# Performance work log

Hardware: AMD Instinct MI355X
Metric: run time of the kernel (lower is better)

## Reference

```python
import jax, jax.numpy as jnp
import numpy as np

L = 64      # system size
H = 64      # hiddenSize
IN = 4      # inputDim (POVM)
B = 4096    # batch of configurations


def _make_w(k, din, dout):
    # Padded block-triangular weight: W[idx, i, j, s] is nonzero only for j >= idx,
    # matching Dense(features=(L-idx)*dout) output scattered into rows idx: of h.
    W = jax.random.normal(k, (L, din, L, dout), dtype=jnp.float32) / jnp.sqrt(jnp.float32(din))
    mask = (jnp.arange(L)[:, None] <= jnp.arange(L)[None, :]).astype(jnp.float32)  # [idx, j]
    return W * mask[:, None, :, None]


def setup_inputs() -> dict:
    key = jax.random.key(0)
    ks = jax.random.split(key, 7)
    x = jax.random.randint(ks[0], (B, L), 0, IN, dtype=jnp.int32)
    W0 = _make_w(ks[1], IN, H)
    W1 = _make_w(ks[2], H, H)
    W2 = _make_w(ks[3], H, 4)
    # bias exists only for site idx==0; its (L*size,) output reshaped to (L, size)
    # is added to all rows of h, so it acts as the initial value of h[d].
    b0 = 0.1 * jax.random.normal(ks[4], (L, H), dtype=jnp.float32)
    b1 = 0.1 * jax.random.normal(ks[5], (L, H), dtype=jnp.float32)
    b2 = 0.1 * jax.random.normal(ks[6], (L, 4), dtype=jnp.float32)
    return {"x": x, "W0": W0, "W1": W1, "W2": W2, "b0": b0, "b1": b1, "b2": b2}


def reference(x, W0, W1, W2, b0, b1, b2):
    Bn = x.shape[0]
    x_oh = jax.nn.one_hot(x, IN, dtype=jnp.float32)                      # (B, L, 4)
    # ffn_cell input: one-hot of x[:-1], shifted right with a zero row prepended
    x_in = jnp.concatenate([jnp.zeros((Bn, 1, IN), jnp.float32), x_oh[:, :-1]], axis=1)

    h0 = jnp.broadcast_to(b0, (Bn, L, H))
    h1 = jnp.broadcast_to(b1, (Bn, L, H))
    h2 = jnp.broadcast_to(b2, (Bn, L, 4))

    def step(carry, inp):
        h0, h1, h2 = carry
        a, idx, w0, w1, w2 = inp                                        # a: (B, 4)
        h0 = h0 + jnp.einsum('bi,ijs->bjs', a, w0)                      # scatter-add rows >= idx
        a = jax.nn.elu(jnp.take(h0, idx, axis=1))                       # (B, H)
        h1 = h1 + jnp.einsum('bi,ijs->bjs', a, w1)
        a = jax.nn.elu(jnp.take(h1, idx, axis=1))
        h2 = h2 + jnp.einsum('bi,ijs->bjs', a, w2)
        return (h0, h1, h2), None

    xs = (jnp.swapaxes(x_in, 0, 1), jnp.arange(L), W0, W1, W2)
    (h0, h1, h2), _ = jax.lax.scan(step, (h0, h1, h2), xs)

    out = jax.nn.elu(h2)                                                # (B, L, 4)
    logp = jnp.sum(jax.nn.log_softmax(out, axis=-1) * x_oh, axis=(1, 2))
    return logp                                                         # (B,)
```

## Files before the change

kernel.cpp:

```cpp
#include <hip/hip_runtime.h>
#include <hip/hip_bf16.h>

#define LL 64
#define HH 64
#define KDIM 4096

typedef __attribute__((ext_vector_type(8))) short bf16x8;
typedef __attribute__((ext_vector_type(4))) short s16x4;
typedef __attribute__((ext_vector_type(4))) float f32x4;

__device__ inline short f2bf(float f) {
    __hip_bfloat16 h = __float2bfloat16(f);
    return *reinterpret_cast<short*>(&h);
}
__device__ inline float elu1(float x) { return x > 0.f ? x : expm1f(x); }

__device__ inline void global_load_lds16(const short* g, short* l) {
    __builtin_amdgcn_global_load_lds(
        (const __attribute__((address_space(1))) unsigned int*)g,
        (__attribute__((address_space(3))) unsigned int*)l,
        16, 0, 0);
}

__global__ __launch_bounds__(256) void k_transpose_cvt(
    const float* __restrict__ in, short* __restrict__ out, int R, int C,
    int skip_margin)
{
    __shared__ float tile[32][33];
    int tx = threadIdx.x & 31, ty = threadIdx.x >> 5;
    size_t r0 = (size_t)blockIdx.y * 32, c0 = (size_t)blockIdx.x * 32;
    if (skip_margin >= 0 && (int)r0 >= (int)c0 + skip_margin) return;
#pragma unroll
    for (int i = 0; i < 32; i += 8)
        tile[ty + i][tx] = in[(r0 + ty + i) * C + (c0 + tx)];
    __syncthreads();
#pragma unroll
    for (int i = 0; i < 32; i += 8)
        out[(c0 + ty + i) * R + (r0 + tx)] = f2bf(tile[tx][ty + i]);
}

__global__ __launch_bounds__(256) void k_onehot(
    const int* __restrict__ x, short* __restrict__ Xoh)
{
    int b = blockIdx.x * 4 + (threadIdx.x >> 6);
    int t = threadIdx.x & 63;
    s16x4 v = {0, 0, 0, 0};
    if (t > 0) {
        int xi = x[b * LL + t - 1];
        v[xi] = (short)0x3F80;
    }
    *(s16x4*)(Xoh + (size_t)b * 256 + t * 4) = v;
}

template<int SHIFT, bool OUT_BF16>
__global__ __launch_bounds__(256) void k_gemm_bt(
    const short* __restrict__ A,
    const short* __restrict__ BT,
    const float* __restrict__ bias,
    void* __restrict__ Cv,
    int M, int N, int K)
{
    constexpr int BM = 128, BN = 128, BK = 32;
    __shared__ short As[BM * BK];
    __shared__ short Bs[BN * BK];

    int m0 = blockIdx.x * BM;
    int n0 = ((int)gridDim.y - 1 - (int)blockIdx.y) * BN;
    int tid = threadIdx.x;
    int wave = tid >> 6, lane = tid & 63;
    int wm = (wave >> 1) * 64, wn = (wave & 1) * 64;

    int ke;
    if constexpr (SHIFT >= 0) ke = (n0 + BN) << SHIFT;
    else                      ke = (n0 + BN) >> (-SHIFT);
    int k_end = min(K, ke);

    f32x4 acc[4][4] = {};

    int rsub = lane >> 2;
    int csub = (lane & 3) * 8;
    const short* ga = A  + (size_t)(m0 + wave * 16 + rsub) * K + csub;
    const short* gb = BT + (size_t)(n0 + wave * 16 + rsub) * K + csub;
    short* lA = &As[(wave * 16) * BK];
    short* lB = &Bs[(wave * 16) * BK];

    int lrow = lane & 15;
    int lko  = (lane >> 4) * 8;
    const short* rA = &As[(wm + lrow) * BK + lko];
    const short* rB = &Bs[(wn + lrow) * BK + lko];

    for (int kb = 0; kb < k_end; kb += BK) {
        __syncthreads();
        global_load_lds16(ga + kb,                  lA);
        global_load_lds16(ga + kb + (size_t)64 * K, lA + 64 * BK);
        global_load_lds16(gb + kb,                  lB);
        global_load_lds16(gb + kb + (size_t)64 * K, lB + 64 * BK);
        __syncthreads();

        bf16x8 af[4], bf[4];
#pragma unroll
        for (int i = 0; i < 4; ++i) {
            af[i] = *(const bf16x8*)(rA + i * 16 * BK);
            bf[i] = *(const bf16x8*)(rB + i * 16 * BK);
        }
#pragma unroll
        for (int mi = 0; mi < 4; ++mi)
#pragma unroll
            for (int ni = 0; ni < 4; ++ni)
                acc[mi][ni] = __builtin_amdgcn_mfma_f32_16x16x32_bf16(
                    af[mi], bf[ni], acc[mi][ni], 0, 0, 0);
    }

    int lcol = lane & 15;
    int lr4  = (lane >> 4) * 4;
#pragma unroll
    for (int mi = 0; mi < 4; ++mi) {
#pragma unroll
        for (int ni = 0; ni < 4; ++ni) {
            int col = n0 + wn + ni * 16 + lcol;
            float bv = bias[col];
#pragma unroll
            for (int r = 0; r < 4; ++r) {
                int row = m0 + wm + mi * 16 + lr4 + r;
                float v = elu1(acc[mi][ni][r] + bv);
                if (OUT_BF16) ((short*)Cv)[(size_t)row * N + col] = f2bf(v);
                else          ((float*)Cv)[(size_t)row * N + col] = v;
            }
        }
    }
}

template<int SHIFT, int ZSPLIT>
__global__ __launch_bounds__(256) void k_gemm_bt_splitk(
    const short* __restrict__ A, const short* __restrict__ BT,
    float* __restrict__ part, int M, int N, int K)
{
    constexpr int BM = 128, BN = 128, BK = 32;
    __shared__ short As[BM * BK];
    __shared__ short Bs[BN * BK];

    int m0 = blockIdx.x * BM;
    int n0 = ((int)gridDim.y - 1 - (int)blockIdx.y) * BN;
    int z = blockIdx.z;
    int tid = threadIdx.x;
    int wave = tid >> 6, lane = tid & 63;
    int wm = (wave >> 1) * 64, wn = (wave & 1) * 64;

    int k_end = min(K, (n0 + BN) << SHIFT);
    int chunk = ((k_end / ZSPLIT + BK - 1) / BK) * BK;
    int kb0 = z * chunk;
    int kb1 = min(k_end, kb0 + chunk);

    f32x4 acc[4][4] = {};

    int rsub = lane >> 2;
    int csub = (lane & 3) * 8;
    const short* ga = A  + (size_t)(m0 + wave * 16 + rsub) * K + csub;
    const short* gb = BT + (size_t)(n0 + wave * 16 + rsub) * K + csub;
    short* lA = &As[(wave * 16) * BK];
    short* lB = &Bs[(wave * 16) * BK];

    int lrow = lane & 15;
    int lko  = (lane >> 4) * 8;
    const short* rA = &As[(wm + lrow) * BK + lko];
    const short* rB = &Bs[(wn + lrow) * BK + lko];

    for (int kb = kb0; kb < kb1; kb += BK) {
        __syncthreads();
        global_load_lds16(ga + kb,                  lA);
        global_load_lds16(ga + kb + (size_t)64 * K, lA + 64 * BK);
        global_load_lds16(gb + kb,                  lB);
        global_load_lds16(gb + kb + (size_t)64 * K, lB + 64 * BK);
        __syncthreads();

        bf16x8 af[4], bf[4];
#pragma unroll
        for (int i = 0; i < 4; ++i) {
            af[i] = *(const bf16x8*)(rA + i * 16 * BK);
            bf[i] = *(const bf16x8*)(rB + i * 16 * BK);
        }
#pragma unroll
        for (int mi = 0; mi < 4; ++mi)
#pragma unroll
            for (int ni = 0; ni < 4; ++ni)
                acc[mi][ni] = __builtin_amdgcn_mfma_f32_16x16x32_bf16(
                    af[mi], bf[ni], acc[mi][ni], 0, 0, 0);
    }

    float* p = part + (size_t)z * M * N;
    int lcol = lane & 15;
    int lr4  = (lane >> 4) * 4;
#pragma unroll
    for (int mi = 0; mi < 4; ++mi)
#pragma unroll
        for (int ni = 0; ni < 4; ++ni) {
            int col = n0 + wn + ni * 16 + lcol;
#pragma unroll
            for (int r = 0; r < 4; ++r) {
                int row = m0 + wm + mi * 16 + lr4 + r;
                p[(size_t)row * N + col] = acc[mi][ni][r];
            }
        }
}

__global__ __launch_bounds__(256) void k_logp_fused(
    const float* __restrict__ part, const float* __restrict__ b2,
    const int* __restrict__ x, float* __restrict__ logp)
{
    const size_t MN = (size_t)4096 * 256;
    int b = blockIdx.x * 4 + (threadIdx.x >> 6);
    int j = threadIdx.x & 63;
    size_t idx = (size_t)b * 256 + j * 4;

    f32x4 o = *(const f32x4*)(part + idx);
    f32x4 p1 = *(const f32x4*)(part + idx + MN);
    f32x4 p2 = *(const f32x4*)(part + idx + 2 * MN);
    f32x4 p3 = *(const f32x4*)(part + idx + 3 * MN);
    f32x4 bv = *(const f32x4*)(b2 + j * 4);
#pragma unroll
    for (int s = 0; s < 4; ++s)
        o[s] = elu1(o[s] + p1[s] + p2[s] + p3[s] + bv[s]);

    float m = fmaxf(fmaxf(o[0], o[1]), fmaxf(o[2], o[3]));
    float lse = m + logf(expf(o[0] - m) + expf(o[1] - m) +
                         expf(o[2] - m) + expf(o[3] - m));
    int xi = x[b * LL + j];
    float sel = (xi == 0) ? o[0] : (xi == 1) ? o[1] : (xi == 2) ? o[2] : o[3];
    float c = sel - lse;
#pragma unroll
    for (int off = 32; off > 0; off >>= 1)
        c += __shfl_down(c, off, 64);
    if (j == 0) logp[b] = c;
}

extern "C" void kernel_launch(void* const* d_in, const int* in_sizes, int n_in,
                              void* d_out, int out_size, void* d_ws, size_t ws_size,
                              hipStream_t stream)
{
    const int*   x  = (const int*)  d_in[0];
    const float* W0 = (const float*)d_in[1];
    const float* W1 = (const float*)d_in[2];
    const float* W2 = (const float*)d_in[3];
    const float* b0 = (const float*)d_in[4];
    const float* b1 = (const float*)d_in[5];
    const float* b2 = (const float*)d_in[6];
    float* logp = (float*)d_out;

    char* ws = (char*)d_ws;
    short* W1T  = (short*)(ws);
    short* W2T  = (short*)(ws + (size_t)33554432);
    short* W0T  = (short*)(ws + (size_t)35651584);
    short* Xoh  = (short*)(ws + (size_t)37748736);
    short* A1   = (short*)(ws + (size_t)39845888);
    float* part = (float*)(ws + (size_t)39845888);
    short* A2   = (short*)(ws + (size_t)73400320);

    k_transpose_cvt<<<dim3(128, 128), 256, 0, stream>>>(W1, W1T, 4096, 4096, 160);
    k_transpose_cvt<<<dim3(8, 128),   256, 0, stream>>>(W2, W2T, 4096, 256, -1);
    k_transpose_cvt<<<dim3(128, 8),   256, 0, stream>>>(W0, W0T, 256, 4096, -1);

    k_onehot<<<1024, 256, 0, stream>>>(x, Xoh);

    k_gemm_bt<-4, true><<<dim3(32, 32), 256, 0, stream>>>(Xoh, W0T, b0, A1, 4096, 4096, 256);

    k_gemm_bt<0, true><<<dim3(32, 32), 256, 0, stream>>>(A1, W1T, b1, A2, 4096, 4096, 4096);

    k_gemm_bt_splitk<4, 4><<<dim3(32, 2, 4), 256, 0, stream>>>(A2, W2T, part, 4096, 256, 4096);

    k_logp_fused<<<1024, 256, 0, stream>>>(part, b2, x, logp);
}
```

Measured before the change: 182.7 us.

## Merge weight transposes into one launch and interleave triangular GEMM tile order

Replaces the three transpose-convert kernel launches with one launch that splits its flat block index across W1, W2 and W0, which removes per-launch overhead and tail gaps. It also remaps the GEMM's N-tile ordering through tri_map, interleaving heavy and light column tiles of the triangular workload so that concurrently scheduled blocks have more even K ranges. The remap only takes effect when the grid's y-dimension is a multiple of 8, and it adds integer division to each block's setup.

```diff
diff --git a/kernel.cpp b/kernel.cpp
--- a/kernel.cpp
+++ b/kernel.cpp
@@ -22,14 +22,38 @@
         16, 0, 0);
 }
 
-__global__ __launch_bounds__(256) void k_transpose_cvt(
-    const float* __restrict__ in, short* __restrict__ out, int R, int C,
-    int skip_margin)
-{
+__device__ inline int tri_map(int yy, int gy) {
+    if ((gy & 7) == 0) {
+        int q = gy >> 2, i = yy / q, r = yy % q;
+        return (i == 0) ? r
+             : (i == 1) ? (gy / 2 - 1 - r)
+             : (i == 2) ? (gy / 2 + r)
+                        : (gy - 1 - r);
+    }
+    return gy - 1 - yy;
+}
+
+__global__ __launch_bounds__(256) void k_transpose_all(
+    const float* __restrict__ W1, short* __restrict__ W1T,
+    const float* __restrict__ W2, short* __restrict__ W2T,
+    const float* __restrict__ W0, short* __restrict__ W0T)
+{
+    const float* in; short* out; int R, C, bx, by;
+    int bid = blockIdx.x;
+    if (bid < 16384) {
+        bx = bid & 127; by = bid >> 7;
+        if (by * 32 >= bx * 32 + 160) return;
+        in = W1; out = W1T; R = 4096; C = 4096;
+    } else if (bid < 17408) {
+        int id = bid - 16384; bx = id & 7; by = id >> 3;
+        in = W2; out = W2T; R = 4096; C = 256;
+    } else {
+        int id = bid - 17408; bx = id & 127; by = id >> 7;
+        in = W0; out = W0T; R = 256; C = 4096;
+    }
     __shared__ float tile[32][33];
     int tx = threadIdx.x & 31, ty = threadIdx.x >> 5;
-    size_t r0 = (size_t)blockIdx.y * 32, c0 = (size_t)blockIdx.x * 32;
-    if (skip_margin >= 0 && (int)r0 >= (int)c0 + skip_margin) return;
+    size_t r0 = (size_t)by * 32, c0 = (size_t)bx * 32;
 #pragma unroll
     for (int i = 0; i < 32; i += 8)
         tile[ty + i][tx] = in[(r0 + ty + i) * C + (c0 + tx)];
@@ -65,7 +89,7 @@
     __shared__ short Bs[BN * BK];
 
     int m0 = blockIdx.x * BM;
-    int n0 = ((int)gridDim.y - 1 - (int)blockIdx.y) * BN;
+    int n0 = tri_map(blockIdx.y, gridDim.y) * BN;
     int tid = threadIdx.x;
     int wave = tid >> 6, lane = tid & 63;
     int wm = (wave >> 1) * 64, wn = (wave & 1) * 64;
@@ -255,9 +279,7 @@
     float* part = (float*)(ws + (size_t)39845888);
     short* A2   = (short*)(ws + (size_t)73400320);
 
-    k_transpose_cvt<<<dim3(128, 128), 256, 0, stream>>>(W1, W1T, 4096, 4096, 160);
-    k_transpose_cvt<<<dim3(8, 128),   256, 0, stream>>>(W2, W2T, 4096, 256, -1);
-    k_transpose_cvt<<<dim3(128, 8),   256, 0, stream>>>(W0, W0T, 256, 4096, -1);
+    k_transpose_all<<<18432, 256, 0, stream>>>(W1, W1T, W2, W2T, W0, W0T);
 
     k_onehot<<<1024, 256, 0, stream>>>(x, Xoh);
 
```

Measured after the change: 190.9 us. 4.5% more time.
